# Optimization experiments

Hardware: AMD Instinct MI355X
Metric: run time of the kernel (lower is better)

Reference implementation:

```python
import jax, jax.numpy as jnp
import numpy as np

E = 16      # num_experts
H = 1024    # hidden_dim
I = 2048    # intermediate_dim
K = 2       # top_k routing
T = 2048    # tokens


def setup_inputs() -> dict:
    key = jax.random.key(0)
    k0, k1, k2, k3, k4 = jax.random.split(key, 5)
    std = 0.02  # nn.init.normal_(std=0.02) in _create_new_expert
    return {
        "x": jax.random.normal(k0, (T, H), dtype=jnp.float32),
        "w_router": jax.random.normal(k1, (H, E), dtype=jnp.float32) * std,
        "w_gate": jax.random.normal(k2, (E, H, I), dtype=jnp.float32) * std,
        "w_up": jax.random.normal(k3, (E, H, I), dtype=jnp.float32) * std,
        "w_down": jax.random.normal(k4, (E, I, H), dtype=jnp.float32) * std,
    }


def reference(x, w_router, w_gate, w_up, w_down):
    # --- router: softmax gating, top-k selection, renormalized weights ---
    logits = x @ w_router                                   # [T, E]
    probs = jax.nn.softmax(logits, axis=-1)                 # [T, E]
    vals, idx = jax.lax.top_k(probs, K)                     # [T, K]
    vals = vals / jnp.sum(vals, axis=-1, keepdims=True)     # renormalize over top-k
    # sparse combine weights: zero outside selected experts  [T, E]
    combine = jnp.sum(jax.nn.one_hot(idx, E, dtype=x.dtype) * vals[..., None], axis=1)
    # --- per-expert SwiGLU FFN (dense-over-experts, masked combine) ---
    gate = jnp.einsum('th,ehi->tei', x, w_gate)             # [T, E, I]
    up = jnp.einsum('th,ehi->tei', x, w_up)                 # [T, E, I]
    hidden = jax.nn.silu(gate) * up * combine[:, :, None]   # fuse combine weight
    y = jnp.einsum('tei,eih->th', hidden, w_down)           # [T, H]
    return y
```

## Files before the change

kernel.cpp:

```cpp
#include <hip/hip_runtime.h>
#include <hip/hip_bf16.h>
#include <math.h>


#define T_TOK 2048
#define H_DIM 1024
#define I_DIM 2048
#define E_NUM 16
#define N_ASSIGN 4096
#define BM 128
#define TILE_MAX 48

typedef __attribute__((ext_vector_type(8))) short short8;
typedef __attribute__((ext_vector_type(4))) float floatx4;

#define WS_OFF_COUNTS   0
#define WS_OFF_OFFSETS  64
#define WS_OFF_TOPKIDX  256
#define WS_OFF_TOPKW    (WS_OFF_TOPKIDX + 16384)
#define WS_OFF_ROWTOK   (WS_OFF_TOPKW  + 16384)
#define WS_OFF_ROWW     (WS_OFF_ROWTOK + 16384)
#define WS_OFF_TILEE    (WS_OFF_ROWW   + 16384)
#define WS_OFF_TILEM    (WS_OFF_TILEE  + 256)
#define WS_OFF_TILEC    (WS_OFF_TILEM  + 256)
#define WS_OFF_XG       (128 * 1024)
#define WS_OFF_H1       (WS_OFF_XG + 8u * 1024 * 1024)

__device__ __forceinline__ ushort f2bf(float f) {
    union { float f; unsigned int u; } v; v.f = f;
    unsigned int r = (v.u + 0x7fffu + ((v.u >> 16) & 1u)) >> 16;
    return (ushort)r;
}

#define FENCE_LGKM0() asm volatile("s_waitcnt lgkmcnt(0)" ::: "memory")
#define WAIT_VM(N)    asm volatile("s_waitcnt vmcnt(" #N ")" ::: "memory")
#define BARRIER_()                                    \
    do {                                              \
        FENCE_LGKM0();                                \
        __builtin_amdgcn_s_barrier();                 \
        asm volatile("" ::: "memory");                \
    } while (0)

__global__ __launch_bounds__(64)
void router_kernel(const float* __restrict__ x,
                   const float* __restrict__ wr,
                   int* __restrict__ counts,
                   int* __restrict__ topk_idx,
                   float* __restrict__ topk_w) {
    const int t = blockIdx.x;
    const int lane = threadIdx.x;
    const float* xt = x + (size_t)t * H_DIM;

    float acc[E_NUM];
#pragma unroll
    for (int e = 0; e < E_NUM; e++) acc[e] = 0.f;

    for (int h = lane; h < H_DIM; h += 64) {
        const float xv = xt[h];
        const float* wrow = wr + h * E_NUM;
#pragma unroll
        for (int e = 0; e < E_NUM; e++) acc[e] += xv * wrow[e];
    }
#pragma unroll
    for (int off = 32; off > 0; off >>= 1) {
#pragma unroll
        for (int e = 0; e < E_NUM; e++)
            acc[e] += __shfl_down(acc[e], off);
    }
    if (lane == 0) {
        int e0 = 0; float l0 = acc[0];
        for (int e = 1; e < E_NUM; e++)
            if (acc[e] > l0) { l0 = acc[e]; e0 = e; }
        int e1 = (e0 == 0) ? 1 : 0;
        float l1 = acc[e1];
        for (int e = 0; e < E_NUM; e++)
            if (e != e0 && acc[e] > l1) { l1 = acc[e]; e1 = e; }
        const float w0 = 1.f / (1.f + __expf(l1 - l0));
        const float w1 = 1.f - w0;
        topk_idx[t * 2 + 0] = e0;
        topk_idx[t * 2 + 1] = e1;
        topk_w[t * 2 + 0] = w0;
        topk_w[t * 2 + 1] = w1;
        atomicAdd(&counts[e0], 1);
        atomicAdd(&counts[e1], 1);
    }
}

__global__ __launch_bounds__(256)
void scatter_kernel(const int* __restrict__ counts,
                    int* __restrict__ offsets,
                    const int* __restrict__ topk_idx,
                    const float* __restrict__ topk_w,
                    int* __restrict__ row_token,
                    float* __restrict__ row_w,
                    int* __restrict__ tile_e,
                    int* __restrict__ tile_m,
                    int* __restrict__ tile_c) {
    __shared__ int base[E_NUM];
    __shared__ int fill[E_NUM];
    const int tid = threadIdx.x;
    if (tid == 0) {
        int run = 0, tc = 0;
        for (int e = 0; e < E_NUM; e++) {
            offsets[e] = run;
            base[e] = run;
            const int cnt = counts[e];
            run += cnt;
            for (int m = 0; m * BM < cnt; m++) {
                tile_e[tc] = e;
                tile_m[tc] = m;
                tc++;
            }
        }
        offsets[E_NUM] = run;
        *tile_c = tc;
    }
    if (tid < E_NUM) fill[tid] = 0;
    __syncthreads();
    for (int a = tid; a < N_ASSIGN; a += blockDim.x) {
        const int e = topk_idx[a];
        const int pos = atomicAdd(&fill[e], 1);
        const int dst = base[e] + pos;
        row_token[dst] = a >> 1;
        row_w[dst] = topk_w[a];
    }
}

__global__ __launch_bounds__(256)
void gather_x_kernel(const float* __restrict__ x,
                     const int* __restrict__ row_token,
                     ushort* __restrict__ Xg) {
    const int r = blockIdx.x;
    const int t = row_token[r];
    const int c = threadIdx.x;
    floatx4 v = ((const floatx4*)(x + (size_t)t * H_DIM))[c];
    ushort4 o;
    o.x = f2bf(v[0]); o.y = f2bf(v[1]); o.z = f2bf(v[2]); o.w = f2bf(v[3]);
    ((ushort4*)(Xg + (size_t)r * H_DIM))[c] = o;
}

__global__ __launch_bounds__(256)
void gemm_gu_kernel(const ushort* __restrict__ Xg,
                    const float* __restrict__ wg,
                    const float* __restrict__ wu,
                    const int* __restrict__ offsets,
                    const float* __restrict__ row_w,
                    const int* __restrict__ tile_e,
                    const int* __restrict__ tile_m,
                    const int* __restrict__ tile_c,
                    ushort* __restrict__ h1) {
    if ((int)blockIdx.y >= *tile_c) return;
    const int e     = tile_e[blockIdx.y];
    const int mtile = tile_m[blockIdx.y];
    const int ntile = blockIdx.x;
    const int beg = offsets[e];
    const int n   = offsets[e + 1] - beg;

    __shared__ ushort As[2][BM * 32];
    __shared__ ushort Bgs[2][64 * 40];
    __shared__ ushort Bus[2][64 * 40];
    __shared__ float  wts[BM];

    const int tid  = threadIdx.x;
    const int lane = tid & 63;
    const int w    = tid >> 6;
    const int ml   = lane & 15;
    const int q    = lane >> 4;
    const int rq   = (ml >> 1) & 3;
    const int srcq = (lane & 3) ^ ((lane >> 3) & 3);

    if (tid < BM) {
        const int rl = mtile * BM + tid;
        wts[tid] = (rl < n) ? row_w[beg + rl] : 0.f;
    }

    floatx4 accg[2][4], accu[2][4];
#pragma unroll
    for (int i = 0; i < 2; i++)
#pragma unroll
        for (int j = 0; j < 4; j++) {
            accg[i][j] = (floatx4){0.f, 0.f, 0.f, 0.f};
            accu[i][j] = (floatx4){0.f, 0.f, 0.f, 0.f};
        }

    const ushort* Ap[2];
#pragma unroll
    for (int j = 0; j < 2; j++) {
        int row = beg + mtile * BM + 32 * w + 16 * j + (lane >> 2);
        row = row < 4095 ? row : 4095;
        Ap[j] = Xg + (size_t)row * H_DIM + srcq * 8;
    }

    const int kh = tid & 15;
    const int n4 = tid >> 4;
    const float* Bgp = wg + (size_t)e * H_DIM * I_DIM + ntile * 64 + n4 * 4;
    const float* Bup = wu + (size_t)e * H_DIM * I_DIM + ntile * 64 + n4 * 4;

    floatx4 g0p, g1p, u0p, u1p, g0q, g1q, u0q, u1q;

#define GU_ISSUE_A(k0v, buf)                                                   \
    {                                                                          \
        __builtin_amdgcn_global_load_lds(                                      \
            (const __attribute__((address_space(1))) unsigned int*)(Ap[0] + (k0v)), \
            (__attribute__((address_space(3))) unsigned int*)(&As[buf][(32 * w) * 32]), \
            16, 0, 0);                                                         \
        __builtin_amdgcn_global_load_lds(                                      \
            (const __attribute__((address_space(1))) unsigned int*)(Ap[1] + (k0v)), \
            (__attribute__((address_space(3))) unsigned int*)(&As[buf][(32 * w + 16) * 32]), \
            16, 0, 0);                                                         \
    }

#define GU_ISSUE_B(k0v, G0, G1, U0, U1)                                        \
    {                                                                          \
        const size_t boff = (size_t)((k0v) + 2 * kh) * I_DIM;                  \
        G0 = *(const floatx4*)(Bgp + boff);                                    \
        G1 = *(const floatx4*)(Bgp + boff + I_DIM);                            \
        U0 = *(const floatx4*)(Bup + boff);                                    \
        U1 = *(const floatx4*)(Bup + boff + I_DIM);                            \
    }

#define GU_CVT_B(buf, G0, G1, U0, U1)                                          \
    {                                                                          \
        _Pragma("unroll")                                                      \
        for (int j2 = 0; j2 < 4; j2++) {                                       \
            unsigned int pg = (unsigned int)f2bf(G0[j2]) |                     \
                              ((unsigned int)f2bf(G1[j2]) << 16);              \
            unsigned int pu = (unsigned int)f2bf(U0[j2]) |                     \
                              ((unsigned int)f2bf(U1[j2]) << 16);              \
            *(unsigned int*)&Bgs[buf][(n4 * 4 + j2) * 40 + 2 * kh] = pg;       \
            *(unsigned int*)&Bus[buf][(n4 * 4 + j2) * 40 + 2 * kh] = pu;       \
        }                                                                      \
    }

    GU_ISSUE_B(0, g0p, g1p, u0p, u1p);
    GU_ISSUE_A(0, 0);
    GU_ISSUE_B(32, g0q, g1q, u0q, u1q);
    GU_ISSUE_A(32, 1);
    WAIT_VM(6);
    GU_CVT_B(0, g0p, g1p, u0p, u1p);
    BARRIER_();

#define GU_STEP(cur, kpre, CG0, CG1, CU0, CU1, PG0, PG1, PU0, PU1)             \
    {                                                                          \
        short8 af[2], bgf[4], buf4[4];                                         \
        _Pragma("unroll")                                                      \
        for (int mt = 0; mt < 2; mt++)                                         \
            af[mt] = *(const short8*)&As[cur][(32 * w + mt * 16 + ml) * 32 +   \
                                              ((q ^ rq) * 8)];                 \
        FENCE_LGKM0();             \
        GU_ISSUE_B(kpre, PG0, PG1, PU0, PU1);                                  \
        GU_ISSUE_A(kpre, cur);                                                 \
        _Pragma("unroll")                                                      \
        for (int nt = 0; nt < 4; nt++) {                                       \
            bgf[nt]  = *(const short8*)&Bgs[cur][(nt * 16 + ml) * 40 + q * 8]; \
            buf4[nt] = *(const short8*)&Bus[cur][(nt * 16 + ml) * 40 + q * 8]; \
        }                                                                      \
        __builtin_amdgcn_s_setprio(1);                                         \
        _Pragma("unroll")                                                      \
        for (int mt = 0; mt < 2; mt++)                                         \
            _Pragma("unroll")                                                  \
            for (int nt = 0; nt < 4; nt++) {                                   \
                accg[mt][nt] = __builtin_amdgcn_mfma_f32_16x16x32_bf16(        \
                    af[mt], bgf[nt], accg[mt][nt], 0, 0, 0);                   \
                accu[mt][nt] = __builtin_amdgcn_mfma_f32_16x16x32_bf16(        \
                    af[mt], buf4[nt], accu[mt][nt], 0, 0, 0);                  \
            }                                                                  \
        __builtin_amdgcn_s_setprio(0);                                         \
        WAIT_VM(6);                                                            \
        GU_CVT_B(cur ^ 1, CG0, CG1, CU0, CU1);                                 \
        BARRIER_();                                                            \
    }

    for (int k0 = 0; k0 < H_DIM; k0 += 64) {
        const int kpe = (k0 + 64) & (H_DIM - 1);
        const int kpo = (k0 + 96) & (H_DIM - 1);
        GU_STEP(0, kpe, g0q, g1q, u0q, u1q, g0p, g1p, u0p, u1p);
        GU_STEP(1, kpo, g0p, g1p, u0p, u1p, g0q, g1q, u0q, u1q);
    }
#undef GU_STEP
#undef GU_CVT_B
#undef GU_ISSUE_B
#undef GU_ISSUE_A

#pragma unroll
    for (int mt = 0; mt < 2; mt++)
#pragma unroll
        for (int r = 0; r < 4; r++) {
            const int rloc = 32 * w + mt * 16 + q * 4 + r;
            const int rl = mtile * BM + rloc;
            if (rl < n) {
                const float cw = wts[rloc];
#pragma unroll
                for (int nt = 0; nt < 4; nt++) {
                    const float g = accg[mt][nt][r];
                    const float s = g / (1.f + __expf(-g));
                    h1[(size_t)(beg + rl) * I_DIM + ntile * 64 + nt * 16 + ml] =
                        f2bf(s * accu[mt][nt][r] * cw);
                }
            }
        }
}

__global__ __launch_bounds__(256)
void gemm_down_kernel(const ushort* __restrict__ h1,
                      const float* __restrict__ wd,
                      const int* __restrict__ offsets,
                      const int* __restrict__ row_token,
                      const int* __restrict__ tile_e,
                      const int* __restrict__ tile_m,
                      const int* __restrict__ tile_c,
                      float* __restrict__ y) {
    if ((int)blockIdx.y >= *tile_c) return;
    const int e     = tile_e[blockIdx.y];
    const int mtile = tile_m[blockIdx.y];
    const int ntile = blockIdx.x;
    const int kbase = blockIdx.z * 1024;
    const int beg = offsets[e];
    const int n   = offsets[e + 1] - beg;

    __shared__ ushort As[2][BM * 32];
    __shared__ ushort Bs[2][64 * 40];
    __shared__ int    toks[BM];

    const int tid  = threadIdx.x;
    const int lane = tid & 63;
    const int w    = tid >> 6;
    const int ml   = lane & 15;
    const int q    = lane >> 4;
    const int rq   = (ml >> 1) & 3;
    const int srcq = (lane & 3) ^ ((lane >> 3) & 3);

    if (tid < BM) {
        const int rl = mtile * BM + tid;
        toks[tid] = (rl < n) ? row_token[beg + rl] : 0;
    }

    floatx4 acc[2][4];
#pragma unroll
    for (int i = 0; i < 2; i++)
#pragma unroll
        for (int j = 0; j < 4; j++) acc[i][j] = (floatx4){0.f, 0.f, 0.f, 0.f};

    const ushort* Ap[2];
#pragma unroll
    for (int j = 0; j < 2; j++) {
        int row = beg + mtile * BM + 32 * w + 16 * j + (lane >> 2);
        row = row < 4095 ? row : 4095;
        Ap[j] = h1 + (size_t)row * I_DIM + kbase + srcq * 8;
    }

    const int kh = tid & 15;
    const int n4 = tid >> 4;
    const float* Bp = wd + (size_t)e * I_DIM * H_DIM +
                      (size_t)kbase * H_DIM + ntile * 64 + n4 * 4;

    floatx4 b0p, b1p, b0q, b1q;

#define D_ISSUE_A(k0v, buf)                                                    \
    {                                                                          \
        __builtin_amdgcn_global_load_lds(                                      \
            (const __attribute__((address_space(1))) unsigned int*)(Ap[0] + (k0v)), \
            (__attribute__((address_space(3))) unsigned int*)(&As[buf][(32 * w) * 32]), \
            16, 0, 0);                                                         \
        __builtin_amdgcn_global_load_lds(                                      \
            (const __attribute__((address_space(1))) unsigned int*)(Ap[1] + (k0v)), \
            (__attribute__((address_space(3))) unsigned int*)(&As[buf][(32 * w + 16) * 32]), \
            16, 0, 0);                                                         \
    }

#define D_ISSUE_B(k0v, B0, B1)                                                 \
    {                                                                          \
        const size_t boff = (size_t)((k0v) + 2 * kh) * H_DIM;                  \
        B0 = *(const floatx4*)(Bp + boff);                                     \
        B1 = *(const floatx4*)(Bp + boff + H_DIM);                             \
    }

#define D_CVT_B(buf, B0, B1)                                                   \
    {                                                                          \
        _Pragma("unroll")                                                      \
        for (int j2 = 0; j2 < 4; j2++) {                                       \
            unsigned int p = (unsigned int)f2bf(B0[j2]) |                      \
                             ((unsigned int)f2bf(B1[j2]) << 16);               \
            *(unsigned int*)&Bs[buf][(n4 * 4 + j2) * 40 + 2 * kh] = p;         \
        }                                                                      \
    }

    D_ISSUE_B(0, b0p, b1p);
    D_ISSUE_A(0, 0);
    D_ISSUE_B(32, b0q, b1q);
    D_ISSUE_A(32, 1);
    WAIT_VM(4);
    D_CVT_B(0, b0p, b1p);
    BARRIER_();

#define D_STEP(cur, kpre, CB0, CB1, PB0, PB1)                                  \
    {                                                                          \
        short8 af[2], bfr[4];                                                  \
        _Pragma("unroll")                                                      \
        for (int mt = 0; mt < 2; mt++)                                         \
            af[mt] = *(const short8*)&As[cur][(32 * w + mt * 16 + ml) * 32 +   \
                                              ((q ^ rq) * 8)];                 \
        FENCE_LGKM0();                                                         \
        D_ISSUE_B(kpre, PB0, PB1);                                             \
        D_ISSUE_A(kpre, cur);                                                  \
        _Pragma("unroll")                                                      \
        for (int nt = 0; nt < 4; nt++)                                         \
            bfr[nt] = *(const short8*)&Bs[cur][(nt * 16 + ml) * 40 + q * 8];   \
        __builtin_amdgcn_s_setprio(1);                                         \
        _Pragma("unroll")                                                      \
        for (int mt = 0; mt < 2; mt++)                                         \
            _Pragma("unroll")                                                  \
            for (int nt = 0; nt < 4; nt++)                                     \
                acc[mt][nt] = __builtin_amdgcn_mfma_f32_16x16x32_bf16(         \
                    af[mt], bfr[nt], acc[mt][nt], 0, 0, 0);                    \
        __builtin_amdgcn_s_setprio(0);                                         \
        WAIT_VM(4);                                                            \
        D_CVT_B(cur ^ 1, CB0, CB1);                                            \
        BARRIER_();                                                            \
    }

    for (int k0 = 0; k0 < 1024; k0 += 64) {
        const int kpe = (k0 + 64) & 1023;
        const int kpo = (k0 + 96) & 1023;
        D_STEP(0, kpe, b0q, b1q, b0p, b1p);
        D_STEP(1, kpo, b0p, b1p, b0q, b1q);
    }
#undef D_STEP
#undef D_CVT_B
#undef D_ISSUE_B
#undef D_ISSUE_A

#pragma unroll
    for (int mt = 0; mt < 2; mt++)
#pragma unroll
        for (int r = 0; r < 4; r++) {
            const int rloc = 32 * w + mt * 16 + q * 4 + r;
            const int rl = mtile * BM + rloc;
            if (rl < n) {
                const int t = toks[rloc];
#pragma unroll
                for (int nt = 0; nt < 4; nt++)
                    atomicAdd(&y[(size_t)t * H_DIM + ntile * 64 + nt * 16 + ml],
                              acc[mt][nt][r]);
            }
        }
}

extern "C" void kernel_launch(void* const* d_in, const int* in_sizes, int n_in,
                              void* d_out, int out_size, void* d_ws, size_t ws_size,
                              hipStream_t stream) {
    const float* x  = (const float*)d_in[0];
    const float* wr = (const float*)d_in[1];
    const float* wg = (const float*)d_in[2];
    const float* wu = (const float*)d_in[3];
    const float* wd = (const float*)d_in[4];
    float* y = (float*)d_out;

    char* ws = (char*)d_ws;
    int*    counts    = (int*)(ws + WS_OFF_COUNTS);
    int*    offsets   = (int*)(ws + WS_OFF_OFFSETS);
    int*    topk_idx  = (int*)(ws + WS_OFF_TOPKIDX);
    float*  topk_w    = (float*)(ws + WS_OFF_TOPKW);
    int*    row_token = (int*)(ws + WS_OFF_ROWTOK);
    float*  row_w     = (float*)(ws + WS_OFF_ROWW);
    int*    tile_e    = (int*)(ws + WS_OFF_TILEE);
    int*    tile_m    = (int*)(ws + WS_OFF_TILEM);
    int*    tile_c    = (int*)(ws + WS_OFF_TILEC);
    ushort* Xg        = (ushort*)(ws + WS_OFF_XG);
    ushort* h1        = (ushort*)(ws + WS_OFF_H1);

    hipMemsetAsync(counts, 0, 64, stream);
    hipMemsetAsync(y, 0, (size_t)T_TOK * H_DIM * sizeof(float), stream);

    router_kernel<<<T_TOK, 64, 0, stream>>>(x, wr, counts, topk_idx, topk_w);
    scatter_kernel<<<1, 256, 0, stream>>>(counts, offsets, topk_idx, topk_w,
                                          row_token, row_w, tile_e, tile_m, tile_c);
    gather_x_kernel<<<N_ASSIGN, 256, 0, stream>>>(x, row_token, Xg);
    gemm_gu_kernel<<<dim3(I_DIM / 64, TILE_MAX), 256, 0, stream>>>(
        Xg, wg, wu, offsets, row_w, tile_e, tile_m, tile_c, h1);
    gemm_down_kernel<<<dim3(H_DIM / 64, TILE_MAX, 2), 256, 0, stream>>>(
        h1, wd, offsets, row_token, tile_e, tile_m, tile_c, y);
}
```

Baseline: 579.7 us.

## Replace down-proj atomics with per-row partial buffer and combine kernel; use packed bf16 cvt

The down-projection kernel now covers the full K range in one pass and writes each expert row's output to a per-assignment buffer. A new combine kernel then sums the two expert contributions per token. This removes the float atomicAdd scatter, the split-K over blockIdx.z and the memset of y. The float-to-bf16 conversions are also switched to the packed v_cvt_pk_bf16_f32 instruction. The trade-off is half as many down-GEMM blocks, each doing a longer K loop, plus extra workspace traffic and one more launch.

Result: no change. 581.3 us (+0.3%).

```diff
diff --git a/kernel.cpp b/kernel.cpp
--- a/kernel.cpp
+++ b/kernel.cpp
@@ -23,13 +23,22 @@
 #define WS_OFF_TILEE    (WS_OFF_ROWW   + 16384)
 #define WS_OFF_TILEM    (WS_OFF_TILEE  + 256)
 #define WS_OFF_TILEC    (WS_OFF_TILEM  + 256)
+#define WS_OFF_TOKROWS  (WS_OFF_TILEC  + 64)
 #define WS_OFF_XG       (128 * 1024)
 #define WS_OFF_H1       (WS_OFF_XG + 8u * 1024 * 1024)
+#define WS_OFF_YP       (WS_OFF_H1 + 16u * 1024 * 1024)
+#define WS_NEED_YP      42074112ull
 
 __device__ __forceinline__ ushort f2bf(float f) {
     union { float f; unsigned int u; } v; v.f = f;
     unsigned int r = (v.u + 0x7fffu + ((v.u >> 16) & 1u)) >> 16;
     return (ushort)r;
+}
+
+__device__ __forceinline__ unsigned int cvt_pk_bf16(float lo, float hi) {
+    unsigned int r;
+    asm("v_cvt_pk_bf16_f32 %0, %1, %2" : "=v"(r) : "v"(lo), "v"(hi));
+    return r;
 }
 
 #define FENCE_LGKM0() asm volatile("s_waitcnt lgkmcnt(0)" ::: "memory")
@@ -95,7 +104,8 @@
                     float* __restrict__ row_w,
                     int* __restrict__ tile_e,
                     int* __restrict__ tile_m,
-                    int* __restrict__ tile_c) {
+                    int* __restrict__ tile_c,
+                    int* __restrict__ token_rows) {
     __shared__ int base[E_NUM];
     __shared__ int fill[E_NUM];
     const int tid = threadIdx.x;
@@ -123,6 +133,7 @@
         const int dst = base[e] + pos;
         row_token[dst] = a >> 1;
         row_w[dst] = topk_w[a];
+        token_rows[a] = dst;
     }
 }
 
@@ -134,9 +145,10 @@
     const int t = row_token[r];
     const int c = threadIdx.x;
     floatx4 v = ((const floatx4*)(x + (size_t)t * H_DIM))[c];
-    ushort4 o;
-    o.x = f2bf(v[0]); o.y = f2bf(v[1]); o.z = f2bf(v[2]); o.w = f2bf(v[3]);
-    ((ushort4*)(Xg + (size_t)r * H_DIM))[c] = o;
+    uint2 o;
+    o.x = cvt_pk_bf16(v[0], v[1]);
+    o.y = cvt_pk_bf16(v[2], v[3]);
+    ((uint2*)(Xg + (size_t)r * H_DIM))[c] = o;
 }
 
 __global__ __launch_bounds__(256)
@@ -223,10 +235,8 @@
     {                                                                          \
         _Pragma("unroll")                                                      \
         for (int j2 = 0; j2 < 4; j2++) {                                       \
-            unsigned int pg = (unsigned int)f2bf(G0[j2]) |                     \
-                              ((unsigned int)f2bf(G1[j2]) << 16);              \
-            unsigned int pu = (unsigned int)f2bf(U0[j2]) |                     \
-                              ((unsigned int)f2bf(U1[j2]) << 16);              \
+            unsigned int pg = cvt_pk_bf16(G0[j2], G1[j2]);                     \
+            unsigned int pu = cvt_pk_bf16(U0[j2], U1[j2]);                     \
             *(unsigned int*)&Bgs[buf][(n4 * 4 + j2) * 40 + 2 * kh] = pg;       \
             *(unsigned int*)&Bus[buf][(n4 * 4 + j2) * 40 + 2 * kh] = pu;       \
         }                                                                      \
@@ -301,6 +311,7 @@
         }
 }
 
+template <int USE_YP>
 __global__ __launch_bounds__(256)
 void gemm_down_kernel(const ushort* __restrict__ h1,
                       const float* __restrict__ wd,
@@ -309,12 +320,14 @@
                       const int* __restrict__ tile_e,
                       const int* __restrict__ tile_m,
                       const int* __restrict__ tile_c,
-                      float* __restrict__ y) {
+                      float* __restrict__ y,
+                      float* __restrict__ yp) {
     if ((int)blockIdx.y >= *tile_c) return;
     const int e     = tile_e[blockIdx.y];
     const int mtile = tile_m[blockIdx.y];
     const int ntile = blockIdx.x;
-    const int kbase = blockIdx.z * 1024;
+    const int kbase = USE_YP ? 0 : (int)blockIdx.z * 1024;
+    const int KLEN  = USE_YP ? I_DIM : 1024;
     const int beg = offsets[e];
     const int n   = offsets[e + 1] - beg;
 
@@ -330,7 +343,7 @@
     const int rq   = (ml >> 1) & 3;
     const int srcq = (lane & 3) ^ ((lane >> 3) & 3);
 
-    if (tid < BM) {
+    if (!USE_YP && tid < BM) {
         const int rl = mtile * BM + tid;
         toks[tid] = (rl < n) ? row_token[beg + rl] : 0;
     }
@@ -379,8 +392,7 @@
     {                                                                          \
         _Pragma("unroll")                                                      \
         for (int j2 = 0; j2 < 4; j2++) {                                       \
-            unsigned int p = (unsigned int)f2bf(B0[j2]) |                      \
-                             ((unsigned int)f2bf(B1[j2]) << 16);               \
+            unsigned int p = cvt_pk_bf16(B0[j2], B1[j2]);                      \
             *(unsigned int*)&Bs[buf][(n4 * 4 + j2) * 40 + 2 * kh] = p;         \
         }                                                                      \
     }
@@ -419,9 +431,9 @@
         BARRIER_();                                                            \
     }
 
-    for (int k0 = 0; k0 < 1024; k0 += 64) {
-        const int kpe = (k0 + 64) & 1023;
-        const int kpo = (k0 + 96) & 1023;
+    for (int k0 = 0; k0 < KLEN; k0 += 64) {
+        const int kpe = (k0 + 64) & (KLEN - 1);
+        const int kpo = (k0 + 96) & (KLEN - 1);
         D_STEP(0, kpe, b0q, b1q, b0p, b1p);
         D_STEP(1, kpo, b0p, b1p, b0q, b1q);
     }
@@ -437,13 +449,33 @@
             const int rloc = 32 * w + mt * 16 + q * 4 + r;
             const int rl = mtile * BM + rloc;
             if (rl < n) {
-                const int t = toks[rloc];
-#pragma unroll
-                for (int nt = 0; nt < 4; nt++)
-                    atomicAdd(&y[(size_t)t * H_DIM + ntile * 64 + nt * 16 + ml],
-                              acc[mt][nt][r]);
+                if (USE_YP) {
+#pragma unroll
+                    for (int nt = 0; nt < 4; nt++)
+                        yp[(size_t)(beg + rl) * H_DIM + ntile * 64 + nt * 16 + ml] =
+                            acc[mt][nt][r];
+                } else {
+                    const int t = toks[rloc];
+#pragma unroll
+                    for (int nt = 0; nt < 4; nt++)
+                        atomicAdd(&y[(size_t)t * H_DIM + ntile * 64 + nt * 16 + ml],
+                                  acc[mt][nt][r]);
+                }
             }
         }
+}
+
+__global__ __launch_bounds__(256)
+void combine_kernel(const float* __restrict__ yp,
+                    const int* __restrict__ token_rows,
+                    float* __restrict__ y) {
+    const int t = blockIdx.x;
+    const int c = threadIdx.x;
+    const int r0 = token_rows[2 * t];
+    const int r1 = token_rows[2 * t + 1];
+    floatx4 a = ((const floatx4*)(yp + (size_t)r0 * H_DIM))[c];
+    floatx4 b = ((const floatx4*)(yp + (size_t)r1 * H_DIM))[c];
+    ((floatx4*)(y + (size_t)t * H_DIM))[c] = a + b;
 }
 
 extern "C" void kernel_launch(void* const* d_in, const int* in_sizes, int n_in,
@@ -466,18 +498,30 @@
     int*    tile_e    = (int*)(ws + WS_OFF_TILEE);
     int*    tile_m    = (int*)(ws + WS_OFF_TILEM);
     int*    tile_c    = (int*)(ws + WS_OFF_TILEC);
+    int*    token_rows= (int*)(ws + WS_OFF_TOKROWS);
     ushort* Xg        = (ushort*)(ws + WS_OFF_XG);
     ushort* h1        = (ushort*)(ws + WS_OFF_H1);
+    float*  yp        = (float*)(ws + WS_OFF_YP);
+
+    const bool use_yp = ws_size >= WS_NEED_YP;
 
     hipMemsetAsync(counts, 0, 64, stream);
-    hipMemsetAsync(y, 0, (size_t)T_TOK * H_DIM * sizeof(float), stream);
+    if (!use_yp)
+        hipMemsetAsync(y, 0, (size_t)T_TOK * H_DIM * sizeof(float), stream);
 
     router_kernel<<<T_TOK, 64, 0, stream>>>(x, wr, counts, topk_idx, topk_w);
     scatter_kernel<<<1, 256, 0, stream>>>(counts, offsets, topk_idx, topk_w,
-                                          row_token, row_w, tile_e, tile_m, tile_c);
+                                          row_token, row_w, tile_e, tile_m, tile_c,
+                                          token_rows);
     gather_x_kernel<<<N_ASSIGN, 256, 0, stream>>>(x, row_token, Xg);
     gemm_gu_kernel<<<dim3(I_DIM / 64, TILE_MAX), 256, 0, stream>>>(
         Xg, wg, wu, offsets, row_w, tile_e, tile_m, tile_c, h1);
-    gemm_down_kernel<<<dim3(H_DIM / 64, TILE_MAX, 2), 256, 0, stream>>>(
-        h1, wd, offsets, row_token, tile_e, tile_m, tile_c, y);
-}
+    if (use_yp) {
+        gemm_down_kernel<1><<<dim3(H_DIM / 64, TILE_MAX), 256, 0, stream>>>(
+            h1, wd, offsets, row_token, tile_e, tile_m, tile_c, y, yp);
+        combine_kernel<<<T_TOK, 256, 0, stream>>>(yp, token_rows, y);
+    } else {
+        gemm_down_kernel<0><<<dim3(H_DIM / 64, TILE_MAX, 2), 256, 0, stream>>>(
+            h1, wd, offsets, row_token, tile_e, tile_m, tile_c, y, yp);
+    }
+}
```
